# Kernel tuning notes

Hardware: AMD Instinct MI355X
Metric: run time of the kernel (lower is better)

## Reference

```python
import math
import jax, jax.numpy as jnp
import numpy as np

EMBED_DIM = 1024
NUM_HEADS = 16
HEAD_DIM = EMBED_DIM // NUM_HEADS
B, S = 4, 2048


def setup_inputs() -> dict:
    key = jax.random.key(0)
    ks = jax.random.split(key, 12)
    sc = 1.0 / math.sqrt(EMBED_DIM)
    inp = {
        "query": jax.random.normal(ks[0], (B, S, EMBED_DIM), jnp.float32),
        "key": jax.random.normal(ks[1], (B, S, EMBED_DIM), jnp.float32),
        "value": jax.random.normal(ks[2], (B, S, EMBED_DIM), jnp.float32),
        # causal mask: True = masked (upper triangle above diagonal)
        "attn_mask": jnp.triu(jnp.ones((S, S), jnp.bool_), k=1),
        "q_w": jax.random.normal(ks[3], (EMBED_DIM, EMBED_DIM), jnp.float32) * sc,
        "q_b": jax.random.normal(ks[4], (EMBED_DIM,), jnp.float32) * sc,
        "k_w": jax.random.normal(ks[5], (EMBED_DIM, EMBED_DIM), jnp.float32) * sc,
        "k_b": jax.random.normal(ks[6], (EMBED_DIM,), jnp.float32) * sc,
        "v_w": jax.random.normal(ks[7], (EMBED_DIM, EMBED_DIM), jnp.float32) * sc,
        "v_b": jax.random.normal(ks[8], (EMBED_DIM,), jnp.float32) * sc,
        "o_w": jax.random.normal(ks[9], (EMBED_DIM, EMBED_DIM), jnp.float32) * sc,
        "o_b": jax.random.normal(ks[10], (EMBED_DIM,), jnp.float32) * sc,
    }
    return inp


def _split_heads(x):
    # (B, S, E) -> (B, H, S, D)
    b, s, _ = x.shape
    return x.reshape(b, s, NUM_HEADS, HEAD_DIM).transpose(0, 2, 1, 3)


def reference(query, key, value, attn_mask, q_w, q_b, k_w, k_b, v_w, v_b, o_w, o_b):
    # torch Linear: y = x @ W.T + b
    q = _split_heads(query @ q_w.T + q_b)
    k = _split_heads(key @ k_w.T + k_b)
    v = _split_heads(value @ v_w.T + v_b)
    scale = math.sqrt(HEAD_DIM)
    scores = jnp.einsum("bhqd,bhkd->bhqk", q, k) / scale
    scores = jnp.where(attn_mask[None, None, :, :], -jnp.inf, scores)
    attn = jax.nn.softmax(scores, axis=-1)
    ctx = jnp.einsum("bhqk,bhkd->bhqd", attn, v)  # (B,H,S,D)
    ctx = ctx.transpose(0, 2, 1, 3).reshape(query.shape[0], query.shape[1], EMBED_DIM)
    return ctx @ o_w.T + o_b
```

## Files before the change

kernel.cpp:

```cpp
#include <hip/hip_runtime.h>
#include <stdint.h>

#define BB 4
#define SS 2048
#define EE 1024
#define HH 16
#define DD 64
#define MM (BB*SS)

typedef unsigned short u16;
typedef __attribute__((ext_vector_type(8))) short bf16x8;
typedef __attribute__((ext_vector_type(4))) float f32x4;

#define MFMA __builtin_amdgcn_mfma_f32_16x16x32_bf16

#if __has_builtin(__builtin_amdgcn_exp2f)
#define EXP2(x) __builtin_amdgcn_exp2f(x)
#else
#define EXP2(x) exp2f(x)
#endif

__device__ __forceinline__ u16 f2bf(float f) {
  union { float f; uint32_t u; } x; x.f = f;
  uint32_t r = (x.u + 0x7fffu + ((x.u >> 16) & 1u)) >> 16;
  return (u16)r;
}

__device__ __forceinline__ uint32_t cvtpk(float lo, float hi) {
  uint32_t r;
  asm volatile("v_cvt_pk_bf16_f32 %0, %1, %2" : "=v"(r) : "v"(lo), "v"(hi));
  return r;
}

__device__ __forceinline__ void gl_lds16(const void* g, void* l) {
  __builtin_amdgcn_global_load_lds(
      (const __attribute__((address_space(1))) uint32_t*)g,
      (__attribute__((address_space(3))) uint32_t*)l, 16, 0, 0);
}

__global__ __launch_bounds__(256) void cast_w(
    const float* __restrict__ s0, const float* __restrict__ s1,
    const float* __restrict__ s2, const float* __restrict__ s3,
    u16* __restrict__ d0, u16* __restrict__ d1,
    u16* __restrict__ d2, u16* __restrict__ d3) {
  int i = blockIdx.x * 256 + threadIdx.x;
  int sel = i >> 17, off = i & ((1 << 17) - 1);
  const float* s = sel == 0 ? s0 : sel == 1 ? s1 : sel == 2 ? s2 : s3;
  u16* d = sel == 0 ? d0 : sel == 1 ? d1 : sel == 2 ? d2 : d3;
  const float4* sp = (const float4*)s;
  float4 a = sp[off*2], b = sp[off*2+1];
  union { u16 h[8]; uint4 v; } o;
  o.h[0]=f2bf(a.x); o.h[1]=f2bf(a.y); o.h[2]=f2bf(a.z); o.h[3]=f2bf(a.w);
  o.h[4]=f2bf(b.x); o.h[5]=f2bf(b.y); o.h[6]=f2bf(b.z); o.h[7]=f2bf(b.w);
  *(uint4*)(d + (size_t)off*8) = o.v;
}

template<int A_FP32, int OUT_BF16>
__device__ __forceinline__ void gemm_body(
    const void* __restrict__ Ap, const u16* __restrict__ W,
    const float* __restrict__ bias, void* __restrict__ Cout,
    int Ndim, int Kdim, float scale, int m0, int n0,
    char* AsB, char* BsB) {
  const int tid = threadIdx.x;
  const int lane = tid & 63, w = tid >> 6;
  const int wr = w >> 1, wc = w & 1;
  const int l15 = lane & 15, l4 = lane >> 4;

  f32x4 acc[4][4] = {};

  const int srow = tid >> 2, st = tid & 3;
  const int ssw = st ^ ((srow >> 1) & 3);
  const u16* bg = W + (size_t)(n0 + srow) * Kdim + ssw * 8;
  const size_t rstrideB = (size_t)64 * Kdim;

  const int ar = tid >> 3, asl = tid & 7;
  const int asw = asl ^ (ar & 7);
  const float* agf = nullptr;
  const u16*   agh = nullptr;
  if (A_FP32) agf = (const float*)Ap + (size_t)(m0 + ar) * Kdim + asw * 4;
  else        agh = (const u16*)Ap + (size_t)(m0 + srow) * Kdim + ssw * 8;

  auto stage = [&](int k0, int bi) {
    if (A_FP32) {
      #pragma unroll
      for (int i = 0; i < 4; ++i)
        gl_lds16(agf + (size_t)i*32*Kdim + k0, AsB + bi*16384 + i*4096 + tid*16);
    } else {
      gl_lds16(agh + k0,                    AsB + bi*8192 + tid*16);
      gl_lds16(agh + k0 + (size_t)64*Kdim,  AsB + bi*8192 + 4096 + tid*16);
    }
    gl_lds16(bg + k0,            BsB + bi*8192 + tid*16);
    gl_lds16(bg + k0 + rstrideB, BsB + bi*8192 + 4096 + tid*16);
  };

  stage(0, 0);
  __syncthreads();

  const int T = Kdim / 32;
  for (int t = 0; t < T; ++t) {
    const int bi = t & 1;
    if (t + 1 < T) stage((t + 1) * 32, bi ^ 1);

    bf16x8 af[4], bfr[4];
    #pragma unroll
    for (int m = 0; m < 4; ++m) {
      int r = wr*64 + m*16 + l15;
      if (A_FP32) {
        const char* rb = AsB + bi*16384 + r*128;
        f32x4 fa = *(const f32x4*)(rb + (((l4*2    ) ^ (r & 7)) * 16));
        f32x4 fb = *(const f32x4*)(rb + (((l4*2 + 1) ^ (r & 7)) * 16));
        union { uint32_t u[4]; bf16x8 v; } cv;
        cv.u[0] = cvtpk(fa[0], fa[1]);
        cv.u[1] = cvtpk(fa[2], fa[3]);
        cv.u[2] = cvtpk(fb[0], fb[1]);
        cv.u[3] = cvtpk(fb[2], fb[3]);
        af[m] = cv.v;
      } else {
        af[m] = *(const bf16x8*)(AsB + bi*8192 + r*64 + ((l4 ^ ((r >> 1) & 3)) * 16));
      }
    }
    #pragma unroll
    for (int n = 0; n < 4; ++n) {
      int rr = wc*64 + n*16 + l15;
      bfr[n] = *(const bf16x8*)(BsB + bi*8192 + rr*64 + ((l4 ^ ((rr >> 1) & 3)) * 16));
    }
    #pragma unroll
    for (int m = 0; m < 4; ++m)
      #pragma unroll
      for (int n = 0; n < 4; ++n)
        acc[m][n] = MFMA(af[m], bfr[n], acc[m][n], 0, 0, 0);
    __syncthreads();
  }

  const int ccol = wc*64 + l15;
  float bv[4];
  #pragma unroll
  for (int n = 0; n < 4; ++n) bv[n] = bias[n0 + ccol + n*16];
  #pragma unroll
  for (int m = 0; m < 4; ++m) {
    #pragma unroll
    for (int i = 0; i < 4; ++i) {
      size_t row = (size_t)(m0 + wr*64 + m*16 + l4*4 + i);
      #pragma unroll
      for (int n = 0; n < 4; ++n) {
        float v = (acc[m][n][i] + bv[n]) * scale;
        size_t idx = row * Ndim + (n0 + ccol + n*16);
        if (OUT_BF16) ((u16*)Cout)[idx] = f2bf(v);
        else          ((float*)Cout)[idx] = v;
      }
    }
  }
}

__global__ __launch_bounds__(256, 2) void gemm_qkv(
    const float* __restrict__ qx, const float* __restrict__ kx, const float* __restrict__ vx,
    const u16* __restrict__ wqm, const u16* __restrict__ wkm, const u16* __restrict__ wvm,
    const float* __restrict__ qbv, const float* __restrict__ kbv, const float* __restrict__ vbv,
    u16* __restrict__ qo, u16* __restrict__ ko, u16* __restrict__ vo) {
  __shared__ alignas(16) char AsB[2*16384];
  __shared__ alignas(16) char BsB[2*8192];
  const int flat = blockIdx.x + blockIdx.y * 8 + blockIdx.z * 512;
  const int j = flat & 7, s = flat >> 3;
  const int c = 6*j + (s >> 5), i = s & 31;
  const int nx = i & 7;
  const int my = ((c & 15) << 2) + (i >> 3);
  const int z = c >> 4;
  const float* A = z == 0 ? qx : z == 1 ? kx : vx;
  const u16* W = z == 0 ? wqm : z == 1 ? wkm : wvm;
  const float* bias = z == 0 ? qbv : z == 1 ? kbv : vbv;
  u16* C = z == 0 ? qo : z == 1 ? ko : vo;
  const float scale = z == 0 ? 0.125f : 1.0f;
  gemm_body<1,1>(A, W, bias, C, EE, EE, scale, my * 128, nx * 128, AsB, BsB);
}

__global__ __launch_bounds__(256, 4) void gemm_out(
    const u16* __restrict__ A, const u16* __restrict__ W,
    const float* __restrict__ bias, float* __restrict__ Cout) {
  __shared__ alignas(16) char AsB[2*8192];
  __shared__ alignas(16) char BsB[2*8192];
  const int flat = blockIdx.x + blockIdx.y * 8;
  const int j = flat & 7, s = flat >> 3;
  const int nx = s & 7, yy = (j << 3) + (s >> 3);
  gemm_body<0,0>(A, W, bias, Cout, EE, EE, 1.0f, yy * 128, nx * 128, AsB, BsB);
}

__global__ __launch_bounds__(256, 2) void attn9(
    const u16* __restrict__ Q, const u16* __restrict__ K,
    const u16* __restrict__ V, u16* __restrict__ ctx) {
  __shared__ alignas(16) u16 Ks[2][2][64*64];
  __shared__ alignas(16) u16 VTs[2][2][64*64];
  __shared__ alignas(16) u16 Ps[4][32*64];

  const int tid = threadIdx.x, lane = tid & 63, w = tid >> 6;
  const int l15 = lane & 15, l4 = lane >> 4;

  const int f = blockIdx.x;
  const int j = f & 7, s = f >> 3;
  const int qlo = s & 7;
  const int panel = j * 8 + (s >> 3);
  const int h = panel & 15, b = panel >> 4;
  const size_t base = ((size_t)b * SS) * EE + h * DD;

  const int kr  = tid >> 3;
  const int ksl = tid & 7;
  const int rv  = tid >> 2;
  const int vc  = tid & 3;

  u16* KsE  = (u16*)Ks;
  u16* VTsE = (u16*)VTs;
  u16* PsE  = (u16*)Ps + w * 2048;

  auto stageK = [&](int t, int pb, int sub) {
    #pragma unroll
    for (int i = 0; i < 2; ++i) {
      int row = i*32 + kr;
      gl_lds16(K + base + (size_t)(t*64 + row)*EE + (ksl ^ (row & 7))*8,
               KsE + pb*8192 + sub*4096 + i*2048 + tid*8);
    }
  };
  auto vtWrite = [&](int pb, int sub, bf16x8 v0, bf16x8 v1) {
    #pragma unroll
    for (int jj = 0; jj < 16; ++jj) {
      u16 val = jj < 8 ? (u16)v0[jj] : (u16)v1[jj - 8];
      int d = vc*16 + jj;
      int sl = (rv >> 3) ^ (jj & 7) ^ (vc << 1);
      VTsE[pb*8192 + sub*4096 + d*64 + sl*8 + (rv & 7)] = val;
    }
  };

  #pragma unroll 1
  for (int pass = 0; pass < 2; ++pass) {
    const int qblk = pass == 0 ? (15 - qlo) : qlo;
    const int q0 = qblk * 128, wq = q0 + w * 32;
    const int npairs = qblk + 1;

    bf16x8 qf[2][2];
    #pragma unroll
    for (int G = 0; G < 2; ++G)
      #pragma unroll
      for (int kc = 0; kc < 2; ++kc)
        qf[G][kc] = *(const bf16x8*)(Q + base + (size_t)(wq + G*16 + l15)*EE + kc*32 + l4*8);

    f32x4 o[2][4] = {};
    float lsum[2] = {0.f, 0.f};

    auto computeTile = [&](int t, int pb, int sub) {
      if (wq + 31 < t*64) return;
      const bool g0act = (wq + 15 >= t*64);
      const u16* tileK = KsE + pb*8192 + sub*4096;
      const u16* tileV = VTsE + pb*8192 + sub*4096;

      f32x4 sc[2][4] = {};
      #pragma unroll
      for (int nt = 0; nt < 4; ++nt) {
        int row = nt*16 + l15;
        int sw = row & 7;
        const u16* kb = tileK + row*64;
        bf16x8 kf0 = *(const bf16x8*)(kb + ((l4    ) ^ sw)*8);
        bf16x8 kf1 = *(const bf16x8*)(kb + ((4 + l4) ^ sw)*8);
        sc[1][nt] = MFMA(kf0, qf[1][0], sc[1][nt], 0, 0, 0);
        sc[1][nt] = MFMA(kf1, qf[1][1], sc[1][nt], 0, 0, 0);
        if (g0act) {
          sc[0][nt] = MFMA(kf0, qf[0][0], sc[0][nt], 0, 0, 0);
          sc[0][nt] = MFMA(kf1, qf[0][1], sc[0][nt], 0, 0, 0);
        }
      }

      #pragma unroll
      for (int G = 0; G < 2; ++G) {
        if (G == 0 && !g0act) continue;
        const bool nomask = (t*64 + 63 <= wq + G*16);
        const int qg = wq + G*16 + l15;
        #pragma unroll
        for (int nt = 0; nt < 4; ++nt) {
          float p0 = EXP2(__builtin_fmaf(sc[G][nt][0], 1.44269504f, -17.3123405f));
          float p1 = EXP2(__builtin_fmaf(sc[G][nt][1], 1.44269504f, -17.3123405f));
          float p2 = EXP2(__builtin_fmaf(sc[G][nt][2], 1.44269504f, -17.3123405f));
          float p3 = EXP2(__builtin_fmaf(sc[G][nt][3], 1.44269504f, -17.3123405f));
          if (!nomask) {
            int kvs = t*64 + nt*16 + l4*4;
            if (kvs + 0 > qg) p0 = 0.f;
            if (kvs + 1 > qg) p1 = 0.f;
            if (kvs + 2 > qg) p2 = 0.f;
            if (kvs + 3 > qg) p3 = 0.f;
          }
          lsum[G] += (p0 + p1) + (p2 + p3);
          uint2 pk;
          pk.x = cvtpk(p0, p1);
          pk.y = cvtpk(p2, p3);
          *(uint2*)((char*)PsE + (G*16 + l15)*128
                        + (((nt*2 + (l4 >> 1)) ^ (l15 & 7)) * 16)
                        + (l4 & 1) * 8) = pk;
        }
      }

      #pragma unroll
      for (int cc = 0; cc < 2; ++cc) {
        bf16x8 pf1 = *(const bf16x8*)((char*)PsE + (16 + l15)*128
                                     + (((cc*4 + l4) ^ (l15 & 7)) * 16));
        bf16x8 pf0;
        if (g0act)
          pf0 = *(const bf16x8*)((char*)PsE + l15*128
                                     + (((cc*4 + l4) ^ (l15 & 7)) * 16));
        #pragma unroll
        for (int dm = 0; dm < 4; ++dm) {
          int sl = (cc*4 + l4) ^ (l15 & 7) ^ (dm << 1);
          bf16x8 vfv = *(const bf16x8*)(tileV + (dm*16 + l15)*64 + sl*8);
          o[1][dm] = MFMA(pf1, vfv, o[1][dm], 0, 0, 0);
          if (g0act) o[0][dm] = MFMA(pf0, vfv, o[0][dm], 0, 0, 0);
        }
      }
    };

    {
      const u16* va = V + base + (size_t)rv*EE + vc*16;
      const u16* vb = V + base + (size_t)(64 + rv)*EE + vc*16;
      bf16x8 a0 = *(const bf16x8*)va, a1 = *(const bf16x8*)(va + 8);
      bf16x8 b0 = *(const bf16x8*)vb, b1 = *(const bf16x8*)(vb + 8);
      stageK(0, 0, 0);
      stageK(1, 0, 1);
      vtWrite(0, 0, a0, a1);
      vtWrite(0, 1, b0, b1);
    }
    __syncthreads();

    for (int u = 0; u < npairs; ++u) {
      const int cur = u & 1;
      const bool havenext = (u + 1 < npairs);
      bf16x8 na0, na1, nb0, nb1;
      if (havenext) {
        const u16* va = V + base + (size_t)((2*u+2)*64 + rv)*EE + vc*16;
        const u16* vb = V + base + (size_t)((2*u+3)*64 + rv)*EE + vc*16;
        na0 = *(const bf16x8*)va; na1 = *(const bf16x8*)(va + 8);
        nb0 = *(const bf16x8*)vb; nb1 = *(const bf16x8*)(vb + 8);
        stageK(2*u+2, cur ^ 1, 0);
        stageK(2*u+3, cur ^ 1, 1);
      }

      computeTile(2*u, cur, 0);
      if (havenext) vtWrite(cur ^ 1, 0, na0, na1);
      computeTile(2*u + 1, cur, 1);
      if (havenext) vtWrite(cur ^ 1, 1, nb0, nb1);
      __syncthreads();
    }

    #pragma unroll
    for (int G = 0; G < 2; ++G) {
      float r = lsum[G];
      r += __shfl_xor(r, 16);
      r += __shfl_xor(r, 32);
      lsum[G] = 1.0f / r;
    }

    #pragma unroll
    for (int G = 0; G < 2; ++G)
      #pragma unroll
      for (int i = 0; i < 4; ++i) {
        float invv = __shfl(lsum[G], l4*4 + i);
        size_t roff = base + (size_t)(wq + G*16 + l4*4 + i) * EE;
        #pragma unroll
        for (int dm = 0; dm < 4; ++dm)
          ctx[roff + dm*16 + l15] = f2bf(o[G][dm][i] * invv);
      }
  }
}

extern "C" void kernel_launch(void* const* d_in, const int* in_sizes, int n_in,
                              void* d_out, int out_size, void* d_ws, size_t ws_size,
                              hipStream_t stream) {
  const float* query = (const float*)d_in[0];
  const float* key   = (const float*)d_in[1];
  const float* value = (const float*)d_in[2];
  const float* q_w = (const float*)d_in[4];
  const float* q_b = (const float*)d_in[5];
  const float* k_w = (const float*)d_in[6];
  const float* k_b = (const float*)d_in[7];
  const float* v_w = (const float*)d_in[8];
  const float* v_b = (const float*)d_in[9];
  const float* o_w = (const float*)d_in[10];
  const float* o_b = (const float*)d_in[11];

  char* ws = (char*)d_ws;
  const size_t XB = (size_t)MM * EE * 2;
  const size_t WB = (size_t)EE * EE * 2;
  u16* wq = (u16*)(ws);
  u16* wk = (u16*)(ws + WB);
  u16* wv = (u16*)(ws + 2*WB);
  u16* wo = (u16*)(ws + 3*WB);
  u16* qp = (u16*)(ws + 4*WB);
  u16* kp = (u16*)(ws + 4*WB + XB);
  u16* vp = (u16*)(ws + 4*WB + 2*XB);
  u16* ctxb = (u16*)(ws + 4*WB + 3*XB);

  const int nw8 = EE * EE / 8;
  cast_w<<<4*nw8/256, 256, 0, stream>>>(q_w, k_w, v_w, o_w, wq, wk, wv, wo);

  gemm_qkv<<<dim3(8, 64, 3), 256, 0, stream>>>(
      query, key, value, wq, wk, wv, q_b, k_b, v_b, qp, kp, vp);

  attn9<<<512, 256, 0, stream>>>(qp, kp, vp, ctxb);

  gemm_out<<<dim3(EE/128, MM/128), 256, 0, stream>>>(ctxb, wo, o_b, (float*)d_out);
}
```

Before: 180.4 us.

## Replace double-buffered BK=32 GEMM pipeline with single-buffered BK=64 tiles

The GEMM body drops the two-stage LDS double buffer with 32-wide K steps in favour of a single buffer holding 64-wide K tiles, synchronising after each stage. The swizzle and load mapping are rewritten for the wider rows, and each step issues twice as many MFMAs. This halves the number of loop iterations and barriers. In exchange, global-to-LDS loads no longer overlap with compute, and gemm_out's launch-bounds occupancy hint is lowered from 4 to 2.

```diff
diff --git a/kernel.cpp b/kernel.cpp
--- a/kernel.cpp
+++ b/kernel.cpp
@@ -68,67 +68,78 @@
 
   f32x4 acc[4][4] = {};
 
-  const int srow = tid >> 2, st = tid & 3;
-  const int ssw = st ^ ((srow >> 1) & 3);
-  const u16* bg = W + (size_t)(n0 + srow) * Kdim + ssw * 8;
-  const size_t rstrideB = (size_t)64 * Kdim;
-
-  const int ar = tid >> 3, asl = tid & 7;
-  const int asw = asl ^ (ar & 7);
-  const float* agf = nullptr;
-  const u16*   agh = nullptr;
-  if (A_FP32) agf = (const float*)Ap + (size_t)(m0 + ar) * Kdim + asw * 4;
-  else        agh = (const u16*)Ap + (size_t)(m0 + srow) * Kdim + ssw * 8;
-
-  auto stage = [&](int k0, int bi) {
+  const int br = tid >> 3, bsl = tid & 7;
+  const int ar = tid >> 4, asl = tid & 15;
+
+  auto stage = [&](int k0) {
     if (A_FP32) {
-      #pragma unroll
-      for (int i = 0; i < 4; ++i)
-        gl_lds16(agf + (size_t)i*32*Kdim + k0, AsB + bi*16384 + i*4096 + tid*16);
+      const float* Af = (const float*)Ap;
+      #pragma unroll
+      for (int i = 0; i < 8; ++i) {
+        int row = i*16 + ar;
+        int ss = asl ^ (row & 7);
+        gl_lds16(Af + (size_t)(m0 + row)*Kdim + k0 + ss*4, AsB + i*4096 + tid*16);
+      }
     } else {
-      gl_lds16(agh + k0,                    AsB + bi*8192 + tid*16);
-      gl_lds16(agh + k0 + (size_t)64*Kdim,  AsB + bi*8192 + 4096 + tid*16);
-    }
-    gl_lds16(bg + k0,            BsB + bi*8192 + tid*16);
-    gl_lds16(bg + k0 + rstrideB, BsB + bi*8192 + 4096 + tid*16);
+      const u16* Ah = (const u16*)Ap;
+      #pragma unroll
+      for (int i = 0; i < 4; ++i) {
+        int row = i*32 + br;
+        int ss = bsl ^ (row & 7);
+        gl_lds16(Ah + (size_t)(m0 + row)*Kdim + k0 + ss*8, AsB + i*4096 + tid*16);
+      }
+    }
+    #pragma unroll
+    for (int i = 0; i < 4; ++i) {
+      int row = i*32 + br;
+      int ss = bsl ^ (row & 7);
+      gl_lds16(W + (size_t)(n0 + row)*Kdim + k0 + ss*8, BsB + i*4096 + tid*16);
+    }
   };
 
-  stage(0, 0);
-  __syncthreads();
-
-  const int T = Kdim / 32;
-  for (int t = 0; t < T; ++t) {
-    const int bi = t & 1;
-    if (t + 1 < T) stage((t + 1) * 32, bi ^ 1);
-
-    bf16x8 af[4], bfr[4];
+  for (int k0 = 0; k0 < Kdim; k0 += 64) {
+    stage(k0);
+    __syncthreads();
+
+    bf16x8 af[2][4], bfr[2][4];
     #pragma unroll
     for (int m = 0; m < 4; ++m) {
       int r = wr*64 + m*16 + l15;
       if (A_FP32) {
-        const char* rb = AsB + bi*16384 + r*128;
-        f32x4 fa = *(const f32x4*)(rb + (((l4*2    ) ^ (r & 7)) * 16));
-        f32x4 fb = *(const f32x4*)(rb + (((l4*2 + 1) ^ (r & 7)) * 16));
-        union { uint32_t u[4]; bf16x8 v; } cv;
-        cv.u[0] = cvtpk(fa[0], fa[1]);
-        cv.u[1] = cvtpk(fa[2], fa[3]);
-        cv.u[2] = cvtpk(fb[0], fb[1]);
-        cv.u[3] = cvtpk(fb[2], fb[3]);
-        af[m] = cv.v;
+        const char* rb = AsB + r*256;
+        #pragma unroll
+        for (int kk = 0; kk < 2; ++kk) {
+          f32x4 fa = *(const f32x4*)(rb + (kk*8 + ((l4*2    ) ^ (r & 7)))*16);
+          f32x4 fb = *(const f32x4*)(rb + (kk*8 + ((l4*2 + 1) ^ (r & 7)))*16);
+          union { uint32_t u[4]; bf16x8 v; } cv;
+          cv.u[0] = cvtpk(fa[0], fa[1]);
+          cv.u[1] = cvtpk(fa[2], fa[3]);
+          cv.u[2] = cvtpk(fb[0], fb[1]);
+          cv.u[3] = cvtpk(fb[2], fb[3]);
+          af[kk][m] = cv.v;
+        }
       } else {
-        af[m] = *(const bf16x8*)(AsB + bi*8192 + r*64 + ((l4 ^ ((r >> 1) & 3)) * 16));
+        const char* rb = AsB + r*128;
+        #pragma unroll
+        for (int kk = 0; kk < 2; ++kk)
+          af[kk][m] = *(const bf16x8*)(rb + ((kk*4 + l4) ^ (r & 7))*16);
       }
     }
     #pragma unroll
     for (int n = 0; n < 4; ++n) {
       int rr = wc*64 + n*16 + l15;
-      bfr[n] = *(const bf16x8*)(BsB + bi*8192 + rr*64 + ((l4 ^ ((rr >> 1) & 3)) * 16));
-    }
-    #pragma unroll
-    for (int m = 0; m < 4; ++m)
-      #pragma unroll
-      for (int n = 0; n < 4; ++n)
-        acc[m][n] = MFMA(af[m], bfr[n], acc[m][n], 0, 0, 0);
+      const char* rb = BsB + rr*128;
+      #pragma unroll
+      for (int kk = 0; kk < 2; ++kk)
+        bfr[kk][n] = *(const bf16x8*)(rb + ((kk*4 + l4) ^ (rr & 7))*16);
+    }
+    #pragma unroll
+    for (int kk = 0; kk < 2; ++kk)
+      #pragma unroll
+      for (int m = 0; m < 4; ++m)
+        #pragma unroll
+        for (int n = 0; n < 4; ++n)
+          acc[m][n] = MFMA(af[kk][m], bfr[kk][n], acc[m][n], 0, 0, 0);
     __syncthreads();
   }
 
@@ -157,8 +168,8 @@
     const u16* __restrict__ wqm, const u16* __restrict__ wkm, const u16* __restrict__ wvm,
     const float* __restrict__ qbv, const float* __restrict__ kbv, const float* __restrict__ vbv,
     u16* __restrict__ qo, u16* __restrict__ ko, u16* __restrict__ vo) {
-  __shared__ alignas(16) char AsB[2*16384];
-  __shared__ alignas(16) char BsB[2*8192];
+  __shared__ alignas(16) char AsB[32768];
+  __shared__ alignas(16) char BsB[16384];
   const int flat = blockIdx.x + blockIdx.y * 8 + blockIdx.z * 512;
   const int j = flat & 7, s = flat >> 3;
   const int c = 6*j + (s >> 5), i = s & 31;
@@ -173,11 +184,11 @@
   gemm_body<1,1>(A, W, bias, C, EE, EE, scale, my * 128, nx * 128, AsB, BsB);
 }
 
-__global__ __launch_bounds__(256, 4) void gemm_out(
+__global__ __launch_bounds__(256, 2) void gemm_out(
     const u16* __restrict__ A, const u16* __restrict__ W,
     const float* __restrict__ bias, float* __restrict__ Cout) {
-  __shared__ alignas(16) char AsB[2*8192];
-  __shared__ alignas(16) char BsB[2*8192];
+  __shared__ alignas(16) char AsB[16384];
+  __shared__ alignas(16) char BsB[16384];
   const int flat = blockIdx.x + blockIdx.y * 8;
   const int j = flat & 7, s = flat >> 3;
   const int nx = s & 7, yy = (j << 3) + (s >> 3);
```

Result: faster. 166.5 us (-7.7%).
